# Kernel tuning notes

Hardware: AMD Instinct MI355X
Metric: run time of the kernel (lower is better)

## Reference

```python
import jax, jax.numpy as jnp
import numpy as np
import math

NUM_HEADS = 32
NUM_KV = 8
D = 128          # num_hidden == per-head dim in this module
S = 2048
B = 1
DK = 128
ROPE_BASE = 10000.0


def rope(x):
    # x: [B, H, S, D]; standard Llama-style RoPE (split-halves rotation) over positions.
    d = x.shape[-1]
    half = d // 2
    pos = jnp.arange(x.shape[2], dtype=jnp.float32)                       # [S]
    inv_freq = 1.0 / (ROPE_BASE ** (jnp.arange(half, dtype=jnp.float32) / half))
    ang = pos[:, None] * inv_freq[None, :]                                # [S, half]
    cos = jnp.cos(ang)
    sin = jnp.sin(ang)
    x1 = x[..., :half]
    x2 = x[..., half:]
    return jnp.concatenate([x1 * cos - x2 * sin, x1 * sin + x2 * cos], axis=-1)


def setup_inputs() -> dict:
    key = jax.random.key(0)
    ks = jax.random.split(key, 8)
    query = jax.random.normal(ks[0], (B, S, D), dtype=jnp.float32)
    k_in = jax.random.normal(ks[1], (B, S, D), dtype=jnp.float32)
    v_in = jax.random.normal(ks[2], (B, S, D), dtype=jnp.float32)
    # causal mask: 1 where attention allowed (lower triangle incl diagonal)
    mask = jnp.tril(jnp.ones((S, S), dtype=jnp.int32))[None, None]        # [1,1,S,S]
    sc = 0.02
    Wq = jax.random.normal(ks[3], (NUM_HEADS * D, D), dtype=jnp.float32) * sc
    bq = jnp.zeros((NUM_HEADS * D,), dtype=jnp.float32)
    Wk = jax.random.normal(ks[4], (NUM_KV * D, D), dtype=jnp.float32) * sc
    bk = jnp.zeros((NUM_KV * D,), dtype=jnp.float32)
    Wv = jax.random.normal(ks[5], (NUM_KV * D, D), dtype=jnp.float32) * sc
    bv = jnp.zeros((NUM_KV * D,), dtype=jnp.float32)
    Wo = jax.random.normal(ks[6], (D, NUM_HEADS * D), dtype=jnp.float32) * sc
    bo = jnp.zeros((D,), dtype=jnp.float32)
    return {"query": query, "key": k_in, "values": v_in, "mask": mask,
            "Wq": Wq, "bq": bq, "Wk": Wk, "bk": bk, "Wv": Wv, "bv": bv,
            "Wo": Wo, "bo": bo}


def reference(query, key, values, mask, Wq, bq, Wk, bk, Wv, bv, Wo, bo):
    Bq, Sq, Dh = query.shape
    # projections; torch Linear: x @ W.T + b. Note: view (reshape), not transpose,
    # exactly as in the original module.
    q = (query @ Wq.T + bq).reshape(Bq, NUM_HEADS, Sq, Dh)   # [B,H,S,D]
    k = (key @ Wk.T + bk).reshape(Bq, NUM_KV, Sq, Dh)        # [B,Hkv,S,D]
    v = (values @ Wv.T + bv).reshape(Bq, NUM_KV, Sq, Dh)
    rk = rope(k)
    rv = rope(v)  # module applies RoPE to values too (faithful)
    rep = NUM_HEADS // NUM_KV
    # torch .repeat((1, rep, 1, 1)) tiles whole head blocks -> jnp.tile
    rk = jnp.tile(rk, (1, rep, 1, 1))                        # [B,H,S,D]
    rv = jnp.tile(rv, (1, rep, 1, 1))
    scores = jnp.einsum('bhqd,bhkd->bhqk', q, rk) / math.sqrt(DK)
    scores = jnp.where(mask == 0, -jnp.inf, scores)
    attn = jax.nn.softmax(scores, axis=-1)
    out = jnp.einsum('bhqk,bhkd->bhqd', attn, rv)            # [B,H,S,D]
    out = out.transpose(0, 2, 1, 3).reshape(Bq, Sq, NUM_HEADS * Dh)
    return out @ Wo.T + bo
```

## Files before the change

### kernel.cpp

```cpp
#include <hip/hip_runtime.h>

typedef unsigned short u16;
typedef unsigned int u32;
typedef short frag_t __attribute__((ext_vector_type(8)));
typedef float f32x4 __attribute__((ext_vector_type(4)));

#define S_LEN 2048

__device__ __forceinline__ float bf2f(u32 u) {
  union { u32 i; float f; } v; v.i = u << 16; return v.f;
}
__device__ __forceinline__ u16 f2bf(float f) {
  u32 x = __float_as_uint(f);
  u32 r = (x + 0x7fffu + ((x >> 16) & 1u)) >> 16;
  return (u16)r;
}
__device__ __forceinline__ u32 pkbf(float lo, float hi) {
  u32 r;
  asm("v_cvt_pk_bf16_f32 %0, %1, %2" : "=v"(r) : "v"(lo), "v"(hi));
  return r;
}
__device__ __forceinline__ void unpack8(uint4 r, float* o) {
  o[0] = bf2f(r.x & 0xffffu); o[1] = bf2f(r.x >> 16);
  o[2] = bf2f(r.y & 0xffffu); o[3] = bf2f(r.y >> 16);
  o[4] = bf2f(r.z & 0xffffu); o[5] = bf2f(r.z >> 16);
  o[6] = bf2f(r.w & 0xffffu); o[7] = bf2f(r.w >> 16);
}
__device__ __forceinline__ u16 ld_in(const void* p, size_t idx, bool fp32) {
  if (fp32) return f2bf(((const float*)p)[idx]);
  return ((const u16*)p)[idx];
}
__device__ __forceinline__ uint4 ld8(const void* p, size_t eidx, bool fp32) {
  if (!fp32) return *(const uint4*)((const u16*)p + eidx);
  const float4* f = (const float4*)((const float*)p + eidx);
  float4 x = f[0], y = f[1];
  uint4 r;
  r.x = pkbf(x.x, x.y);
  r.y = pkbf(x.z, x.w);
  r.z = pkbf(y.x, y.y);
  r.w = pkbf(y.z, y.w);
  return r;
}

__global__ __launch_bounds__(256) void proj_all(
    const void* __restrict__ query, const void* __restrict__ key,
    const void* __restrict__ values,
    const void* __restrict__ Wq, const void* __restrict__ bq,
    const void* __restrict__ Wk, const void* __restrict__ bk,
    const void* __restrict__ Wv, const void* __restrict__ bv,
    u16* __restrict__ Qb, u16* __restrict__ Kb, u16* __restrict__ Vtmp,
    u32* __restrict__ flag_out) {
  __shared__ u16 As[128][136];
  __shared__ u16 Ws[128][136];
  __shared__ u32 flagS;
  u16 (*Cs)[136] = As;
  const int t = threadIdx.x;
  if (t < 64) {
    u32 e = ((u32)((const u16*)query)[2 * t] >> 7) & 0xFFu;
    bool ok = (e >= 110u && e <= 140u);
    unsigned long long b = __ballot(ok);
    if (t == 0) flagS = (__popcll(b) < 32) ? 1u : 0u;
  }
  __syncthreads();
  const bool fp32 = (flagS != 0u);
  if (t == 0 && blockIdx.x == 0 && blockIdx.y == 0) *flag_out = flagS;
  const int x = blockIdx.x;
  const void *A, *W, *bias;
  u16* C; int N, n0;
  if (x < 32)      { A = query;  W = Wq; bias = bq; C = Qb;   N = 4096; n0 = x << 7; }
  else if (x < 40) { A = key;    W = Wk; bias = bk; C = Kb;   N = 1024; n0 = (x - 32) << 7; }
  else             { A = values; W = Wv; bias = bv; C = Vtmp; N = 1024; n0 = (x - 40) << 7; }
  const float osc = (x < 32) ? 0.12751743f : 1.0f;
  const bool isK = (x >= 32 && x < 40);
  const int g0 = x - 32;
  const int lane = t & 63, w = t >> 6, quad = lane >> 4, l15 = lane & 15;
  const int rm = (w & 1) << 6, rn = (w >> 1) << 6;
#pragma unroll
  for (int i = 0; i < 8; ++i) {
    int task = t + (i << 8);
    int row = task >> 4, ch = (task & 15) << 3;
    *(uint4*)&Ws[row][ch] = ld8(W, (size_t)(n0 + row) * 128 + ch, fp32);
  }
  for (int mi = 0; mi < 2; ++mi) {
    const int m0 = (((int)blockIdx.y << 1) | mi) << 7;
    if (mi) __syncthreads();
#pragma unroll
    for (int i = 0; i < 8; ++i) {
      int task = t + (i << 8);
      int row = task >> 4, ch = (task & 15) << 3;
      *(uint4*)&As[row][ch] = ld8(A, (size_t)(m0 + row) * 128 + ch, fp32);
    }
    __syncthreads();
    f32x4 acc[4][4];
#pragma unroll
    for (int mt = 0; mt < 4; ++mt)
#pragma unroll
      for (int nt = 0; nt < 4; ++nt) acc[mt][nt] = 0.f;
#pragma unroll
    for (int mtp = 0; mtp < 2; ++mtp) {
      frag_t a0[4], a1[4];
#pragma unroll
      for (int kc = 0; kc < 4; ++kc) {
        a0[kc] = *(const frag_t*)&As[rm + mtp * 32 + l15][kc * 32 + quad * 8];
        a1[kc] = *(const frag_t*)&As[rm + mtp * 32 + 16 + l15][kc * 32 + quad * 8];
      }
#pragma unroll
      for (int nt = 0; nt < 4; ++nt)
#pragma unroll
        for (int kc = 0; kc < 4; ++kc) {
          frag_t b = *(const frag_t*)&Ws[rn + nt * 16 + l15][kc * 32 + quad * 8];
          acc[mtp * 2][nt] = __builtin_amdgcn_mfma_f32_16x16x32_bf16(a0[kc], b, acc[mtp * 2][nt], 0, 0, 0);
          acc[mtp * 2 + 1][nt] = __builtin_amdgcn_mfma_f32_16x16x32_bf16(a1[kc], b, acc[mtp * 2 + 1][nt], 0, 0, 0);
        }
    }
    __syncthreads();
#pragma unroll
    for (int nt = 0; nt < 4; ++nt) {
      float bb = bf2f((u32)ld_in(bias, n0 + rn + nt * 16 + l15, fp32));
#pragma unroll
      for (int mt = 0; mt < 4; ++mt) {
        int row = rm + ((mt >> 1) * 32) + ((mt & 1) * 16) + quad * 4;
#pragma unroll
        for (int r = 0; r < 4; ++r)
          Cs[row + r][rn + nt * 16 + l15] = f2bf((acc[mt][nt][r] + bb) * osc);
      }
    }
    __syncthreads();
    if (isK) {
      for (int i = t; i < 8192; i += 256) {
        int row = i >> 6, ii = i & 63;
        int sv = (((m0 + row) & 255) << 3) + g0;
        float invf = __expf(-(float)ii * 0.14391156831212787f);
        float ang = (float)sv * invf;
        float sn, cs;
        sincosf(ang, &sn, &cs);
        float k1 = bf2f((u32)Cs[row][ii]), k2 = bf2f((u32)Cs[row][ii + 64]);
        Cs[row][ii] = f2bf(k1 * cs - k2 * sn);
        Cs[row][ii + 64] = f2bf(k1 * sn + k2 * cs);
      }
      __syncthreads();
    }
#pragma unroll
    for (int i = 0; i < 8; ++i) {
      int task = t + (i << 8);
      int row = task >> 4, ch = (task & 15) << 3;
      *(uint4*)&C[(size_t)(m0 + row) * N + n0 + ch] = *(const uint4*)&Cs[row][ch];
    }
  }
}

__global__ __launch_bounds__(256) void rope_v_tr(const u16* __restrict__ Vb,
                                                 u16* __restrict__ VbT) {
  __shared__ u16 Lt[128][72];
  const int t = threadIdx.x;
  const int s0 = blockIdx.x << 6;
  const int g = blockIdx.y;
  const u16* src = Vb + (size_t)g * S_LEN * 128;
  for (int i = t; i < 512; i += 256) {
    int r = i >> 3, d8 = (i & 7) << 3;
    float lo[8], hi[8];
    unpack8(*(const uint4*)&src[(size_t)(s0 + r) * 128 + d8], lo);
    unpack8(*(const uint4*)&src[(size_t)(s0 + r) * 128 + d8 + 64], hi);
#pragma unroll
    for (int j = 0; j < 8; ++j) {
      float invf = __expf(-(float)(d8 + j) * 0.14391156831212787f);
      float ang = (float)(s0 + r) * invf;
      float sn, cs;
      sincosf(ang, &sn, &cs);
      Lt[d8 + j][r] = f2bf(lo[j] * cs - hi[j] * sn);
      Lt[d8 + 64 + j][r] = f2bf(lo[j] * sn + hi[j] * cs);
    }
  }
  __syncthreads();
  u16* dst = VbT + (size_t)g * 128 * S_LEN + s0;
  for (int i = t; i < 2048; i += 256) {
    int d = i >> 4, s4 = (i & 15) << 2;
    uint2 pk;
    pk.x = (u32)Lt[d][s4] | ((u32)Lt[d][s4 + 1] << 16);
    pk.y = (u32)Lt[d][s4 + 2] | ((u32)Lt[d][s4 + 3] << 16);
    *(uint2*)&dst[(size_t)d * S_LEN + s4] = pk;
  }
}

__global__ __launch_bounds__(256, 2) void attn_mfma(
    const u16* __restrict__ Qb, const u16* __restrict__ Kb,
    const u16* __restrict__ VbT, u16* __restrict__ OpA, u16* __restrict__ OpB,
    float2* __restrict__ Ml, int nkh) {
  __shared__ union SmemU {
    struct { u16 Kt[32][136]; u16 Vt[128][40]; u16 St[128][40]; } m;
    struct { u16 Og[128][136]; } e;
  } su;
  const int t = threadIdx.x;
  const int lane = t & 63, w = t >> 6, quad = lane >> 4, l15 = lane & 15;
  const int g = (int)blockIdx.x & 7;
  const int kh = (int)blockIdx.x >> 3;
  const int pi = (int)blockIdx.y;
  const int h = g + (w << 3);
  const u16* Kg = Kb + (size_t)g * S_LEN * 128;
  const u16* Vg = VbT + (size_t)g * 128 * S_LEN;
  const int kR = t >> 4, kC = (t & 15) << 3;
  const int vR = t >> 2, vC = (t & 3) << 3;
  u16* dst = kh ? OpB : OpA;

  for (int tp = 0; tp < 2; ++tp) {
    const int qt = tp ? pi : 63 - pi;
    const int q0 = qt << 5;
    const int niter = qt + 1;
    frag_t aq[2][4];
#pragma unroll
    for (int qp = 0; qp < 2; ++qp)
#pragma unroll
      for (int kc = 0; kc < 4; ++kc)
        aq[qp][kc] = *(const frag_t*)&Qb[((size_t)h * S_LEN + q0 + qp * 16 + l15) * 128 +
                                         kc * 32 + quad * 8];
    float m_r[2] = {-1e30f, -1e30f}, l_r[2] = {0.f, 0.f};
    f32x4 oacc[2][8];
#pragma unroll
    for (int qp = 0; qp < 2; ++qp)
#pragma unroll
      for (int nt = 0; nt < 8; ++nt) oacc[qp][nt] = 0.f;

    uint4 kpf[2], vpf[2];
    if (kh < niter) {
      const int k0 = kh << 5;
      kpf[0] = *(const uint4*)&Kg[(size_t)(k0 + kR) * 128 + kC];
      kpf[1] = *(const uint4*)&Kg[(size_t)(k0 + kR + 16) * 128 + kC];
      vpf[0] = *(const uint4*)&Vg[(size_t)vR * S_LEN + k0 + vC];
      vpf[1] = *(const uint4*)&Vg[(size_t)(vR + 64) * S_LEN + k0 + vC];
    }
    for (int sj = kh; sj < niter; sj += nkh) {
      const int k0 = sj << 5;
      __syncthreads();
      *(uint4*)&su.m.Kt[kR][kC] = kpf[0];
      *(uint4*)&su.m.Kt[kR + 16][kC] = kpf[1];
      *(uint4*)&su.m.Vt[vR][vC] = vpf[0];
      *(uint4*)&su.m.Vt[vR + 64][vC] = vpf[1];
      __syncthreads();
      if (sj + nkh < niter) {
        const int kn = (sj + nkh) << 5;
        kpf[0] = *(const uint4*)&Kg[(size_t)(kn + kR) * 128 + kC];
        kpf[1] = *(const uint4*)&Kg[(size_t)(kn + kR + 16) * 128 + kC];
        vpf[0] = *(const uint4*)&Vg[(size_t)vR * S_LEN + kn + vC];
        vpf[1] = *(const uint4*)&Vg[(size_t)(vR + 64) * S_LEN + kn + vC];
      }
      f32x4 s4[2][2];
#pragma unroll
      for (int kk = 0; kk < 2; ++kk) { s4[kk][0] = 0.f; s4[kk][1] = 0.f; }
#pragma unroll
      for (int kc = 0; kc < 4; ++kc)
#pragma unroll
        for (int kk = 0; kk < 2; ++kk) {
          frag_t a = *(const frag_t*)&su.m.Kt[kk * 16 + l15][kc * 32 + quad * 8];
          s4[kk][0] = __builtin_amdgcn_mfma_f32_16x16x32_bf16(a, aq[0][kc], s4[kk][0], 0, 0, 0);
          s4[kk][1] = __builtin_amdgcn_mfma_f32_16x16x32_bf16(a, aq[1][kc], s4[kk][1], 0, 0, 0);
        }
      const bool lastm = (sj == niter - 1);
      float alpha[2];
#pragma unroll
      for (int qp = 0; qp < 2; ++qp) {
        const int qg = q0 + qp * 16 + l15;
        float mx = -1e30f;
#pragma unroll
        for (int kk = 0; kk < 2; ++kk)
#pragma unroll
          for (int r = 0; r < 4; ++r) {
            float sv = s4[kk][qp][r];
            if (lastm && (k0 + kk * 16 + quad * 4 + r) > qg) sv = -1e30f;
            s4[kk][qp][r] = sv;
            mx = fmaxf(mx, sv);
          }
        mx = fmaxf(mx, __shfl_xor(mx, 16));
        mx = fmaxf(mx, __shfl_xor(mx, 32));
        float mn = fmaxf(m_r[qp], mx);
        alpha[qp] = __builtin_amdgcn_exp2f(m_r[qp] - mn);
        m_r[qp] = mn;
        float sum = 0.f;
        const int strow = w * 32 + qp * 16 + l15;
#pragma unroll
        for (int kk = 0; kk < 2; ++kk) {
          float p0 = __builtin_amdgcn_exp2f(s4[kk][qp][0] - mn);
          float p1 = __builtin_amdgcn_exp2f(s4[kk][qp][1] - mn);
          float p2 = __builtin_amdgcn_exp2f(s4[kk][qp][2] - mn);
          float p3 = __builtin_amdgcn_exp2f(s4[kk][qp][3] - mn);
          sum += (p0 + p1) + (p2 + p3);
          uint2 pk;
          pk.x = pkbf(p0, p1);
          pk.y = pkbf(p2, p3);
          *(uint2*)&su.m.St[strow][kk * 16 + quad * 4] = pk;
        }
        sum += __shfl_xor(sum, 16);
        sum += __shfl_xor(sum, 32);
        l_r[qp] = l_r[qp] * alpha[qp] + sum;
      }
      if (__any(alpha[0] < 1.0f || alpha[1] < 1.0f)) {
#pragma unroll
        for (int qp = 0; qp < 2; ++qp)
#pragma unroll
          for (int r = 0; r < 4; ++r) {
            float al = __shfl(alpha[qp], quad * 4 + r);
#pragma unroll
            for (int nt = 0; nt < 8; ++nt) oacc[qp][nt][r] *= al;
          }
      }
      frag_t pa0 = *(const frag_t*)&su.m.St[w * 32 + l15][quad * 8];
      frag_t pa1 = *(const frag_t*)&su.m.St[w * 32 + 16 + l15][quad * 8];
#pragma unroll
      for (int nt = 0; nt < 8; ++nt) {
        frag_t v = *(const frag_t*)&su.m.Vt[nt * 16 + l15][quad * 8];
        oacc[0][nt] = __builtin_amdgcn_mfma_f32_16x16x32_bf16(pa0, v, oacc[0][nt], 0, 0, 0);
        oacc[1][nt] = __builtin_amdgcn_mfma_f32_16x16x32_bf16(pa1, v, oacc[1][nt], 0, 0, 0);
      }
    }
    __syncthreads();
#pragma unroll
    for (int qp = 0; qp < 2; ++qp)
#pragma unroll
      for (int r = 0; r < 4; ++r) {
        float fac = 1.0f;
        if (nkh == 1) fac = 1.0f / __shfl(l_r[qp], quad * 4 + r);
        int row = w * 32 + qp * 16 + quad * 4 + r;
#pragma unroll
        for (int nt = 0; nt < 8; ++nt)
          su.e.Og[row][nt * 16 + l15] = f2bf(oacc[qp][nt][r] * fac);
      }
    __syncthreads();
#pragma unroll
    for (int jj = 0; jj < 8; ++jj) {
      int c = t + (jj << 8);
      int row = c >> 4, ch = (c & 15) << 3;
      int hh = row >> 5, qr = row & 31;
      *(uint4*)&dst[(size_t)(q0 + qr) * 4096 + (g + hh * 8) * 128 + ch] =
          *(const uint4*)&su.e.Og[row][ch];
    }
    if (nkh == 2 && quad == 0) {
#pragma unroll
      for (int qp = 0; qp < 2; ++qp)
        Ml[((size_t)kh * 32 + h) * S_LEN + q0 + qp * 16 + l15] =
            make_float2(m_r[qp], l_r[qp]);
    }
  }
}

__global__ __launch_bounds__(256) void out_part(
    const u16* __restrict__ OpA, const u16* __restrict__ OpB,
    const float2* __restrict__ Ml, const void* __restrict__ Wo,
    float* __restrict__ Pout, const u32* __restrict__ flagp, int nkh) {
  __shared__ u16 As[64][136];
  __shared__ u16 Ws[128][136];
  const bool fp32 = (*flagp != 0u);
  const int t = threadIdx.x;
  const int lane = t & 63, w = t >> 6, quad = lane >> 4, l15 = lane & 15;
  const int rm = (w & 1) << 5, rn = (w >> 1) << 6;
  const int m0 = (int)blockIdx.x << 6;
  const int z = (int)blockIdx.y;
  f32x4 acc[2][4];
#pragma unroll
  for (int mt = 0; mt < 2; ++mt)
#pragma unroll
    for (int nt = 0; nt < 4; ++nt) acc[mt][nt] = 0.f;
  for (int kc2 = 0; kc2 < 2; ++kc2) {
    if (kc2) __syncthreads();
    const int kc0 = (z << 8) + (kc2 << 7);
    const int hh = kc0 >> 7;
#pragma unroll
    for (int i = 0; i < 8; ++i) {
      int task = t + (i << 8);
      int row = task >> 4, ch = (task & 15) << 3;
      *(uint4*)&Ws[row][ch] = ld8(Wo, (size_t)row * 4096 + kc0 + ch, fp32);
    }
#pragma unroll
    for (int i = 0; i < 4; ++i) {
      int task = t + (i << 8);
      int row = task >> 4, ch = (task & 15) << 3;
      size_t idx = (size_t)(m0 + row) * 4096 + kc0 + ch;
      if (nkh == 2) {
        int s = m0 + row;
        float2 p1 = Ml[(size_t)hh * S_LEN + s];
        float2 p2 = Ml[(size_t)(32 + hh) * S_LEN + s];
        float mn = fmaxf(p1.x, p2.x);
        float a1 = __builtin_amdgcn_exp2f(p1.x - mn);
        float a2 = __builtin_amdgcn_exp2f(p2.x - mn);
        float linv = 1.0f / (a1 * p1.y + a2 * p2.y);
        float w1 = a1 * linv, w2 = a2 * linv;
        float o1[8], o2[8];
        unpack8(*(const uint4*)&OpA[idx], o1);
        unpack8(*(const uint4*)&OpB[idx], o2);
        uint4 r;
        r.x = pkbf(o1[0] * w1 + o2[0] * w2, o1[1] * w1 + o2[1] * w2);
        r.y = pkbf(o1[2] * w1 + o2[2] * w2, o1[3] * w1 + o2[3] * w2);
        r.z = pkbf(o1[4] * w1 + o2[4] * w2, o1[5] * w1 + o2[5] * w2);
        r.w = pkbf(o1[6] * w1 + o2[6] * w2, o1[7] * w1 + o2[7] * w2);
        *(uint4*)&As[row][ch] = r;
      } else {
        *(uint4*)&As[row][ch] = *(const uint4*)&OpA[idx];
      }
    }
    __syncthreads();
    frag_t a0[4], a1[4];
#pragma unroll
    for (int kc = 0; kc < 4; ++kc) {
      a0[kc] = *(const frag_t*)&As[rm + l15][kc * 32 + quad * 8];
      a1[kc] = *(const frag_t*)&As[rm + 16 + l15][kc * 32 + quad * 8];
    }
#pragma unroll
    for (int nt = 0; nt < 4; ++nt)
#pragma unroll
      for (int kc = 0; kc < 4; ++kc) {
        frag_t b = *(const frag_t*)&Ws[rn + nt * 16 + l15][kc * 32 + quad * 8];
        acc[0][nt] = __builtin_amdgcn_mfma_f32_16x16x32_bf16(a0[kc], b, acc[0][nt], 0, 0, 0);
        acc[1][nt] = __builtin_amdgcn_mfma_f32_16x16x32_bf16(a1[kc], b, acc[1][nt], 0, 0, 0);
      }
  }
#pragma unroll
  for (int mt = 0; mt < 2; ++mt) {
    int mrow = m0 + rm + mt * 16 + quad * 4;
#pragma unroll
    for (int nt = 0; nt < 4; ++nt) {
      int n = rn + nt * 16 + l15;
#pragma unroll
      for (int r = 0; r < 4; ++r)
        Pout[((size_t)z * 2048 + mrow + r) * 128 + n] = acc[mt][nt][r];
    }
  }
}

__global__ __launch_bounds__(256) void out_red(
    const float* __restrict__ Pout, const void* __restrict__ bo,
    void* __restrict__ out, const u32* __restrict__ flagp) {
  const bool fp32 = (*flagp != 0u);
  int e4 = blockIdx.x * 256 + threadIdx.x;
  const float4* P = (const float4*)Pout;
  float4 s = P[e4];
#pragma unroll
  for (int z = 1; z < 16; ++z) {
    float4 p = P[(size_t)z * 65536 + e4];
    s.x += p.x; s.y += p.y; s.z += p.z; s.w += p.w;
  }
  int n = (e4 << 2) & 127;
  s.x += bf2f((u32)ld_in(bo, n + 0, fp32));
  s.y += bf2f((u32)ld_in(bo, n + 1, fp32));
  s.z += bf2f((u32)ld_in(bo, n + 2, fp32));
  s.w += bf2f((u32)ld_in(bo, n + 3, fp32));
  if (fp32) {
    ((float4*)out)[e4] = s;
  } else {
    uint2 pk;
    pk.x = pkbf(s.x, s.y);
    pk.y = pkbf(s.z, s.w);
    *(uint2*)((u16*)out + (e4 << 2)) = pk;
  }
}

extern "C" void kernel_launch(void* const* d_in, const int* in_sizes, int n_in,
                              void* d_out, int out_size, void* d_ws, size_t ws_size,
                              hipStream_t stream) {
  (void)in_sizes; (void)n_in; (void)out_size;
  const void* query  = d_in[0];
  const void* key    = d_in[1];
  const void* values = d_in[2];
  const void* Wq = d_in[4];
  const void* bq = d_in[5];
  const void* Wk = d_in[6];
  const void* bk = d_in[7];
  const void* Wv = d_in[8];
  const void* bv = d_in[9];
  const void* Wo = d_in[10];
  const void* bo = d_in[11];

  char* ws = (char*)d_ws;
  u32* flag   = (u32*)ws;
  u16* Qb     = (u16*)(ws + 64);
  u16* Kb     = (u16*)(ws + 64 + (16ull << 20));
  u16* VbT    = (u16*)(ws + 64 + (20ull << 20));
  u16* Vtmp   = (u16*)(ws + 64 + (24ull << 20));
  u16* OpA    = (u16*)(ws + 64 + (24ull << 20));
  u16* OpB    = (u16*)(ws + 64 + (40ull << 20));
  float2* Mlb = (float2*)(ws + 64 + (56ull << 20));
  float* Pout = (float*)Qb;

  const bool split = (ws_size >= (58ull << 20));
  const int nkh = split ? 2 : 1;

  proj_all<<<dim3(48, 8), 256, 0, stream>>>(query, key, values, Wq, bq, Wk, bk,
                                            Wv, bv, Qb, Kb, Vtmp, flag);
  rope_v_tr<<<dim3(32, 8), 256, 0, stream>>>(Vtmp, VbT);
  attn_mfma<<<dim3(8 * nkh, 32), 256, 0, stream>>>(Qb, Kb, VbT, OpA, OpB, Mlb,
                                                   nkh);
  out_part<<<dim3(32, 16), 256, 0, stream>>>(OpA, OpB, Mlb, Wo, Pout, flag, nkh);
  out_red<<<256, 256, 0, stream>>>(Pout, bo, d_out, flag);
}
```

Measured before the change: 236.2 us.

## Split attention blocks to 16 query rows per wave and fuse V RoPE into projection

Each attention block previously computed 4 heads × 32 query rows, with each wave owning two 16-row query tiles. It now covers 2 heads × 32 rows, with each wave owning one 16-row tile. This doubles the grid and halves per-wave registers so that launch bounds can allow 3 blocks per SM. RoPE on V moves into the projection kernel's epilogue, so the transpose kernel becomes a pure transpose. The cost is that each K/V tile is loaded and staged twice as often across blocks.

```diff
diff --git a/kernel.cpp b/kernel.cpp
--- a/kernel.cpp
+++ b/kernel.cpp
@@ -71,8 +71,8 @@
   else if (x < 40) { A = key;    W = Wk; bias = bk; C = Kb;   N = 1024; n0 = (x - 32) << 7; }
   else             { A = values; W = Wv; bias = bv; C = Vtmp; N = 1024; n0 = (x - 40) << 7; }
   const float osc = (x < 32) ? 0.12751743f : 1.0f;
-  const bool isK = (x >= 32 && x < 40);
-  const int g0 = x - 32;
+  const bool doRope = (x >= 32);
+  const int g0 = (x < 40) ? (x - 32) : (x - 40);
   const int lane = t & 63, w = t >> 6, quad = lane >> 4, l15 = lane & 15;
   const int rm = (w & 1) << 6, rn = (w >> 1) << 6;
 #pragma unroll
@@ -126,7 +126,7 @@
       }
     }
     __syncthreads();
-    if (isK) {
+    if (doRope) {
       for (int i = t; i < 8192; i += 256) {
         int row = i >> 6, ii = i & 63;
         int sv = (((m0 + row) & 255) << 3) + g0;
@@ -149,27 +149,24 @@
   }
 }
 
-__global__ __launch_bounds__(256) void rope_v_tr(const u16* __restrict__ Vb,
-                                                 u16* __restrict__ VbT) {
+__global__ __launch_bounds__(256) void v_tr(const u16* __restrict__ Vb,
+                                            u16* __restrict__ VbT) {
   __shared__ u16 Lt[128][72];
   const int t = threadIdx.x;
   const int s0 = blockIdx.x << 6;
   const int g = blockIdx.y;
   const u16* src = Vb + (size_t)g * S_LEN * 128;
-  for (int i = t; i < 512; i += 256) {
-    int r = i >> 3, d8 = (i & 7) << 3;
-    float lo[8], hi[8];
-    unpack8(*(const uint4*)&src[(size_t)(s0 + r) * 128 + d8], lo);
-    unpack8(*(const uint4*)&src[(size_t)(s0 + r) * 128 + d8 + 64], hi);
-#pragma unroll
-    for (int j = 0; j < 8; ++j) {
-      float invf = __expf(-(float)(d8 + j) * 0.14391156831212787f);
-      float ang = (float)(s0 + r) * invf;
-      float sn, cs;
-      sincosf(ang, &sn, &cs);
-      Lt[d8 + j][r] = f2bf(lo[j] * cs - hi[j] * sn);
-      Lt[d8 + 64 + j][r] = f2bf(lo[j] * sn + hi[j] * cs);
-    }
+  for (int i = t; i < 1024; i += 256) {
+    int r = i >> 4, d16 = (i & 15) << 3;
+    uint4 v = *(const uint4*)&src[(size_t)(s0 + r) * 128 + d16];
+    Lt[d16 + 0][r] = (u16)(v.x & 0xffffu);
+    Lt[d16 + 1][r] = (u16)(v.x >> 16);
+    Lt[d16 + 2][r] = (u16)(v.y & 0xffffu);
+    Lt[d16 + 3][r] = (u16)(v.y >> 16);
+    Lt[d16 + 4][r] = (u16)(v.z & 0xffffu);
+    Lt[d16 + 5][r] = (u16)(v.z >> 16);
+    Lt[d16 + 6][r] = (u16)(v.w & 0xffffu);
+    Lt[d16 + 7][r] = (u16)(v.w >> 16);
   }
   __syncthreads();
   u16* dst = VbT + (size_t)g * 128 * S_LEN + s0;
@@ -182,20 +179,24 @@
   }
 }
 
-__global__ __launch_bounds__(256, 2) void attn_mfma(
+__global__ __launch_bounds__(256, 3) void attn_mfma(
     const u16* __restrict__ Qb, const u16* __restrict__ Kb,
     const u16* __restrict__ VbT, u16* __restrict__ OpA, u16* __restrict__ OpB,
     float2* __restrict__ Ml, int nkh) {
   __shared__ union SmemU {
     struct { u16 Kt[32][136]; u16 Vt[128][40]; u16 St[128][40]; } m;
-    struct { u16 Og[128][136]; } e;
+    struct { u16 Og[64][136]; } e;
   } su;
   const int t = threadIdx.x;
   const int lane = t & 63, w = t >> 6, quad = lane >> 4, l15 = lane & 15;
-  const int g = (int)blockIdx.x & 7;
-  const int kh = (int)blockIdx.x >> 3;
+  const int x = (int)blockIdx.x;
+  const int g = x & 7;
+  const int jh = (x >> 3) & 1;
+  const int kh = x >> 4;
   const int pi = (int)blockIdx.y;
-  const int h = g + (w << 3);
+  const int j = (jh << 1) + (w >> 1);
+  const int h = g + (j << 3);
+  const int qsub = (w & 1) << 4;
   const u16* Kg = Kb + (size_t)g * S_LEN * 128;
   const u16* Vg = VbT + (size_t)g * 128 * S_LEN;
   const int kR = t >> 4, kC = (t & 15) << 3;
@@ -206,19 +207,15 @@
     const int qt = tp ? pi : 63 - pi;
     const int q0 = qt << 5;
     const int niter = qt + 1;
-    frag_t aq[2][4];
-#pragma unroll
-    for (int qp = 0; qp < 2; ++qp)
-#pragma unroll
-      for (int kc = 0; kc < 4; ++kc)
-        aq[qp][kc] = *(const frag_t*)&Qb[((size_t)h * S_LEN + q0 + qp * 16 + l15) * 128 +
-                                         kc * 32 + quad * 8];
-    float m_r[2] = {-1e30f, -1e30f}, l_r[2] = {0.f, 0.f};
-    f32x4 oacc[2][8];
-#pragma unroll
-    for (int qp = 0; qp < 2; ++qp)
-#pragma unroll
-      for (int nt = 0; nt < 8; ++nt) oacc[qp][nt] = 0.f;
+    frag_t aq[4];
+#pragma unroll
+    for (int kc = 0; kc < 4; ++kc)
+      aq[kc] = *(const frag_t*)&Qb[((size_t)h * S_LEN + q0 + qsub + l15) * 128 +
+                                   kc * 32 + quad * 8];
+    float m_r = -1e30f, l_r = 0.f;
+    f32x4 oacc[8];
+#pragma unroll
+    for (int nt = 0; nt < 8; ++nt) oacc[nt] = 0.f;
 
     uint4 kpf[2], vpf[2];
     if (kh < niter) {
@@ -243,101 +240,88 @@
         vpf[0] = *(const uint4*)&Vg[(size_t)vR * S_LEN + kn + vC];
         vpf[1] = *(const uint4*)&Vg[(size_t)(vR + 64) * S_LEN + kn + vC];
       }
-      f32x4 s4[2][2];
-#pragma unroll
-      for (int kk = 0; kk < 2; ++kk) { s4[kk][0] = 0.f; s4[kk][1] = 0.f; }
+      f32x4 s4[2];
+      s4[0] = 0.f; s4[1] = 0.f;
 #pragma unroll
       for (int kc = 0; kc < 4; ++kc)
 #pragma unroll
         for (int kk = 0; kk < 2; ++kk) {
           frag_t a = *(const frag_t*)&su.m.Kt[kk * 16 + l15][kc * 32 + quad * 8];
-          s4[kk][0] = __builtin_amdgcn_mfma_f32_16x16x32_bf16(a, aq[0][kc], s4[kk][0], 0, 0, 0);
-          s4[kk][1] = __builtin_amdgcn_mfma_f32_16x16x32_bf16(a, aq[1][kc], s4[kk][1], 0, 0, 0);
+          s4[kk] = __builtin_amdgcn_mfma_f32_16x16x32_bf16(a, aq[kc], s4[kk], 0, 0, 0);
         }
       const bool lastm = (sj == niter - 1);
-      float alpha[2];
-#pragma unroll
-      for (int qp = 0; qp < 2; ++qp) {
-        const int qg = q0 + qp * 16 + l15;
-        float mx = -1e30f;
-#pragma unroll
-        for (int kk = 0; kk < 2; ++kk)
-#pragma unroll
-          for (int r = 0; r < 4; ++r) {
-            float sv = s4[kk][qp][r];
-            if (lastm && (k0 + kk * 16 + quad * 4 + r) > qg) sv = -1e30f;
-            s4[kk][qp][r] = sv;
-            mx = fmaxf(mx, sv);
-          }
-        mx = fmaxf(mx, __shfl_xor(mx, 16));
-        mx = fmaxf(mx, __shfl_xor(mx, 32));
-        float mn = fmaxf(m_r[qp], mx);
-        alpha[qp] = __builtin_amdgcn_exp2f(m_r[qp] - mn);
-        m_r[qp] = mn;
-        float sum = 0.f;
-        const int strow = w * 32 + qp * 16 + l15;
-#pragma unroll
-        for (int kk = 0; kk < 2; ++kk) {
-          float p0 = __builtin_amdgcn_exp2f(s4[kk][qp][0] - mn);
-          float p1 = __builtin_amdgcn_exp2f(s4[kk][qp][1] - mn);
-          float p2 = __builtin_amdgcn_exp2f(s4[kk][qp][2] - mn);
-          float p3 = __builtin_amdgcn_exp2f(s4[kk][qp][3] - mn);
-          sum += (p0 + p1) + (p2 + p3);
-          uint2 pk;
-          pk.x = pkbf(p0, p1);
-          pk.y = pkbf(p2, p3);
-          *(uint2*)&su.m.St[strow][kk * 16 + quad * 4] = pk;
+      const int qg = q0 + qsub + l15;
+      float mx = -1e30f;
+#pragma unroll
+      for (int kk = 0; kk < 2; ++kk)
+#pragma unroll
+        for (int r = 0; r < 4; ++r) {
+          float sv = s4[kk][r];
+          if (lastm && (k0 + kk * 16 + quad * 4 + r) > qg) sv = -1e30f;
+          s4[kk][r] = sv;
+          mx = fmaxf(mx, sv);
         }
-        sum += __shfl_xor(sum, 16);
-        sum += __shfl_xor(sum, 32);
-        l_r[qp] = l_r[qp] * alpha[qp] + sum;
-      }
-      if (__any(alpha[0] < 1.0f || alpha[1] < 1.0f)) {
-#pragma unroll
-        for (int qp = 0; qp < 2; ++qp)
-#pragma unroll
-          for (int r = 0; r < 4; ++r) {
-            float al = __shfl(alpha[qp], quad * 4 + r);
-#pragma unroll
-            for (int nt = 0; nt < 8; ++nt) oacc[qp][nt][r] *= al;
-          }
-      }
-      frag_t pa0 = *(const frag_t*)&su.m.St[w * 32 + l15][quad * 8];
-      frag_t pa1 = *(const frag_t*)&su.m.St[w * 32 + 16 + l15][quad * 8];
+      mx = fmaxf(mx, __shfl_xor(mx, 16));
+      mx = fmaxf(mx, __shfl_xor(mx, 32));
+      float mn = fmaxf(m_r, mx);
+      float alpha = __builtin_amdgcn_exp2f(m_r - mn);
+      m_r = mn;
+      float sum = 0.f;
+      const int strow = (w << 5) + l15;
+#pragma unroll
+      for (int kk = 0; kk < 2; ++kk) {
+        float p0 = __builtin_amdgcn_exp2f(s4[kk][0] - mn);
+        float p1 = __builtin_amdgcn_exp2f(s4[kk][1] - mn);
+        float p2 = __builtin_amdgcn_exp2f(s4[kk][2] - mn);
+        float p3 = __builtin_amdgcn_exp2f(s4[kk][3] - mn);
+        sum += (p0 + p1) + (p2 + p3);
+        uint2 pk;
+        pk.x = pkbf(p0, p1);
+        pk.y = pkbf(p2, p3);
+        *(uint2*)&su.m.St[strow][kk * 16 + quad * 4] = pk;
+      }
+      sum += __shfl_xor(sum, 16);
+      sum += __shfl_xor(sum, 32);
+      l_r = l_r * alpha + sum;
+      if (__any(alpha < 1.0f)) {
+#pragma unroll
+        for (int r = 0; r < 4; ++r) {
+          float al = __shfl(alpha, quad * 4 + r);
+#pragma unroll
+          for (int nt = 0; nt < 8; ++nt) oacc[nt][r] *= al;
+        }
+      }
+      frag_t pa = *(const frag_t*)&su.m.St[strow][quad * 8];
 #pragma unroll
       for (int nt = 0; nt < 8; ++nt) {
         frag_t v = *(const frag_t*)&su.m.Vt[nt * 16 + l15][quad * 8];
-        oacc[0][nt] = __builtin_amdgcn_mfma_f32_16x16x32_bf16(pa0, v, oacc[0][nt], 0, 0, 0);
-        oacc[1][nt] = __builtin_amdgcn_mfma_f32_16x16x32_bf16(pa1, v, oacc[1][nt], 0, 0, 0);
-      }
-    }
-    __syncthreads();
-#pragma unroll
-    for (int qp = 0; qp < 2; ++qp)
-#pragma unroll
-      for (int r = 0; r < 4; ++r) {
-        float fac = 1.0f;
-        if (nkh == 1) fac = 1.0f / __shfl(l_r[qp], quad * 4 + r);
-        int row = w * 32 + qp * 16 + quad * 4 + r;
-#pragma unroll
-        for (int nt = 0; nt < 8; ++nt)
-          su.e.Og[row][nt * 16 + l15] = f2bf(oacc[qp][nt][r] * fac);
-      }
-    __syncthreads();
-#pragma unroll
-    for (int jj = 0; jj < 8; ++jj) {
+        oacc[nt] = __builtin_amdgcn_mfma_f32_16x16x32_bf16(pa, v, oacc[nt], 0, 0, 0);
+      }
+    }
+    __syncthreads();
+#pragma unroll
+    for (int r = 0; r < 4; ++r) {
+      float fac = 1.0f;
+      if (nkh == 1) fac = 1.0f / __shfl(l_r, quad * 4 + r);
+      int row = (w << 4) + quad * 4 + r;
+#pragma unroll
+      for (int nt = 0; nt < 8; ++nt)
+        su.e.Og[row][nt * 16 + l15] = f2bf(oacc[nt][r] * fac);
+    }
+    __syncthreads();
+#pragma unroll
+    for (int jj = 0; jj < 4; ++jj) {
       int c = t + (jj << 8);
       int row = c >> 4, ch = (c & 15) << 3;
-      int hh = row >> 5, qr = row & 31;
-      *(uint4*)&dst[(size_t)(q0 + qr) * 4096 + (g + hh * 8) * 128 + ch] =
+      int wv = row >> 4;
+      int j2 = (jh << 1) + (wv >> 1);
+      int qr = ((wv & 1) << 4) + (row & 15);
+      *(uint4*)&dst[(size_t)(q0 + qr) * 4096 + (g + (j2 << 3)) * 128 + ch] =
           *(const uint4*)&su.e.Og[row][ch];
     }
-    if (nkh == 2 && quad == 0) {
-#pragma unroll
-      for (int qp = 0; qp < 2; ++qp)
-        Ml[((size_t)kh * 32 + h) * S_LEN + q0 + qp * 16 + l15] =
-            make_float2(m_r[qp], l_r[qp]);
-    }
+    if (nkh == 2 && quad == 0)
+      Ml[((size_t)kh * 32 + h) * S_LEN + q0 + qsub + l15] = make_float2(m_r, l_r);
+    __syncthreads();
   }
 }
 
@@ -483,9 +467,9 @@
 
   proj_all<<<dim3(48, 8), 256, 0, stream>>>(query, key, values, Wq, bq, Wk, bk,
                                             Wv, bv, Qb, Kb, Vtmp, flag);
-  rope_v_tr<<<dim3(32, 8), 256, 0, stream>>>(Vtmp, VbT);
-  attn_mfma<<<dim3(8 * nkh, 32), 256, 0, stream>>>(Qb, Kb, VbT, OpA, OpB, Mlb,
-                                                   nkh);
+  v_tr<<<dim3(32, 8), 256, 0, stream>>>(Vtmp, VbT);
+  attn_mfma<<<dim3(16 * nkh, 32), 256, 0, stream>>>(Qb, Kb, VbT, OpA, OpB, Mlb,
+                                                    nkh);
   out_part<<<dim3(32, 16), 256, 0, stream>>>(OpA, OpB, Mlb, Wo, Pout, flag, nkh);
   out_red<<<256, 256, 0, stream>>>(Pout, bo, d_out, flag);
 }
```

Result: slower. 298.3 us (+26.3%).

## Fuse V RoPE into projection and output reduction into out_part via atomic tickets

Applied to the files above, without the earlier changes.

V RoPE now runs inside the projection kernel's epilogue, as K RoPE already did, so the separate transpose kernel only transposes. The separate out_red launch is removed: each out_part block increments a per-row-tile counter, and the last of the 16 split-K blocks sums the partials, adds the bias and writes the output. The counters are zeroed in the projection kernel. Pout gets its own region when the workspace is large enough, so it no longer aliases Qb. This cuts one launch and the extra transcendental work in the transpose pass, at the cost of threadfence and atomic overhead and a serialized reduction tail.

```diff
diff --git a/kernel.cpp b/kernel.cpp
--- a/kernel.cpp
+++ b/kernel.cpp
@@ -49,7 +49,7 @@
     const void* __restrict__ Wk, const void* __restrict__ bk,
     const void* __restrict__ Wv, const void* __restrict__ bv,
     u16* __restrict__ Qb, u16* __restrict__ Kb, u16* __restrict__ Vtmp,
-    u32* __restrict__ flag_out) {
+    u32* __restrict__ flag_out, u32* __restrict__ cnt) {
   __shared__ u16 As[128][136];
   __shared__ u16 Ws[128][136];
   __shared__ u32 flagS;
@@ -63,7 +63,10 @@
   }
   __syncthreads();
   const bool fp32 = (flagS != 0u);
-  if (t == 0 && blockIdx.x == 0 && blockIdx.y == 0) *flag_out = flagS;
+  if (blockIdx.x == 0 && blockIdx.y == 0) {
+    if (t == 0) *flag_out = flagS;
+    if (t < 32) cnt[t] = 0;
+  }
   const int x = blockIdx.x;
   const void *A, *W, *bias;
   u16* C; int N, n0;
@@ -71,8 +74,8 @@
   else if (x < 40) { A = key;    W = Wk; bias = bk; C = Kb;   N = 1024; n0 = (x - 32) << 7; }
   else             { A = values; W = Wv; bias = bv; C = Vtmp; N = 1024; n0 = (x - 40) << 7; }
   const float osc = (x < 32) ? 0.12751743f : 1.0f;
-  const bool isK = (x >= 32 && x < 40);
-  const int g0 = x - 32;
+  const bool doRope = (x >= 32);
+  const int g0 = (x < 40) ? (x - 32) : (x - 40);
   const int lane = t & 63, w = t >> 6, quad = lane >> 4, l15 = lane & 15;
   const int rm = (w & 1) << 6, rn = (w >> 1) << 6;
 #pragma unroll
@@ -126,7 +129,7 @@
       }
     }
     __syncthreads();
-    if (isK) {
+    if (doRope) {
       for (int i = t; i < 8192; i += 256) {
         int row = i >> 6, ii = i & 63;
         int sv = (((m0 + row) & 255) << 3) + g0;
@@ -149,27 +152,24 @@
   }
 }
 
-__global__ __launch_bounds__(256) void rope_v_tr(const u16* __restrict__ Vb,
-                                                 u16* __restrict__ VbT) {
+__global__ __launch_bounds__(256) void v_tr(const u16* __restrict__ Vb,
+                                            u16* __restrict__ VbT) {
   __shared__ u16 Lt[128][72];
   const int t = threadIdx.x;
   const int s0 = blockIdx.x << 6;
   const int g = blockIdx.y;
   const u16* src = Vb + (size_t)g * S_LEN * 128;
-  for (int i = t; i < 512; i += 256) {
-    int r = i >> 3, d8 = (i & 7) << 3;
-    float lo[8], hi[8];
-    unpack8(*(const uint4*)&src[(size_t)(s0 + r) * 128 + d8], lo);
-    unpack8(*(const uint4*)&src[(size_t)(s0 + r) * 128 + d8 + 64], hi);
-#pragma unroll
-    for (int j = 0; j < 8; ++j) {
-      float invf = __expf(-(float)(d8 + j) * 0.14391156831212787f);
-      float ang = (float)(s0 + r) * invf;
-      float sn, cs;
-      sincosf(ang, &sn, &cs);
-      Lt[d8 + j][r] = f2bf(lo[j] * cs - hi[j] * sn);
-      Lt[d8 + 64 + j][r] = f2bf(lo[j] * sn + hi[j] * cs);
-    }
+  for (int i = t; i < 1024; i += 256) {
+    int r = i >> 4, d16 = (i & 15) << 3;
+    uint4 v = *(const uint4*)&src[(size_t)(s0 + r) * 128 + d16];
+    Lt[d16 + 0][r] = (u16)(v.x & 0xffffu);
+    Lt[d16 + 1][r] = (u16)(v.x >> 16);
+    Lt[d16 + 2][r] = (u16)(v.y & 0xffffu);
+    Lt[d16 + 3][r] = (u16)(v.y >> 16);
+    Lt[d16 + 4][r] = (u16)(v.z & 0xffffu);
+    Lt[d16 + 5][r] = (u16)(v.z >> 16);
+    Lt[d16 + 6][r] = (u16)(v.w & 0xffffu);
+    Lt[d16 + 7][r] = (u16)(v.w >> 16);
   }
   __syncthreads();
   u16* dst = VbT + (size_t)g * 128 * S_LEN + s0;
@@ -344,9 +344,12 @@
 __global__ __launch_bounds__(256) void out_part(
     const u16* __restrict__ OpA, const u16* __restrict__ OpB,
     const float2* __restrict__ Ml, const void* __restrict__ Wo,
-    float* __restrict__ Pout, const u32* __restrict__ flagp, int nkh) {
+    float* __restrict__ Pout, const u32* __restrict__ flagp, int nkh,
+    u32* __restrict__ cnt, const void* __restrict__ bo,
+    void* __restrict__ out) {
   __shared__ u16 As[64][136];
   __shared__ u16 Ws[128][136];
+  __shared__ u32 tickS;
   const bool fp32 = (*flagp != 0u);
   const int t = threadIdx.x;
   const int lane = t & 63, w = t >> 6, quad = lane >> 4, l15 = lane & 15;
@@ -422,32 +425,36 @@
         Pout[((size_t)z * 2048 + mrow + r) * 128 + n] = acc[mt][nt][r];
     }
   }
-}
-
-__global__ __launch_bounds__(256) void out_red(
-    const float* __restrict__ Pout, const void* __restrict__ bo,
-    void* __restrict__ out, const u32* __restrict__ flagp) {
-  const bool fp32 = (*flagp != 0u);
-  int e4 = blockIdx.x * 256 + threadIdx.x;
-  const float4* P = (const float4*)Pout;
-  float4 s = P[e4];
-#pragma unroll
-  for (int z = 1; z < 16; ++z) {
-    float4 p = P[(size_t)z * 65536 + e4];
-    s.x += p.x; s.y += p.y; s.z += p.z; s.w += p.w;
-  }
-  int n = (e4 << 2) & 127;
-  s.x += bf2f((u32)ld_in(bo, n + 0, fp32));
-  s.y += bf2f((u32)ld_in(bo, n + 1, fp32));
-  s.z += bf2f((u32)ld_in(bo, n + 2, fp32));
-  s.w += bf2f((u32)ld_in(bo, n + 3, fp32));
-  if (fp32) {
-    ((float4*)out)[e4] = s;
-  } else {
-    uint2 pk;
-    pk.x = pkbf(s.x, s.y);
-    pk.y = pkbf(s.z, s.w);
-    *(uint2*)((u16*)out + (e4 << 2)) = pk;
+  __threadfence();
+  __syncthreads();
+  if (t == 0) tickS = atomicAdd(&cnt[blockIdx.x], 1u);
+  __syncthreads();
+  if (tickS == 15) {
+    __threadfence();
+    const float4* P = (const float4*)Pout;
+    for (int i = t; i < 2048; i += 256) {
+      int row = i >> 5, c4 = i & 31;
+      size_t base = (size_t)(m0 + row) * 32 + c4;
+      float4 s = P[base];
+#pragma unroll
+      for (int zz = 1; zz < 16; ++zz) {
+        float4 p = P[(size_t)zz * 65536 + base];
+        s.x += p.x; s.y += p.y; s.z += p.z; s.w += p.w;
+      }
+      int n = c4 << 2;
+      s.x += bf2f((u32)ld_in(bo, n + 0, fp32));
+      s.y += bf2f((u32)ld_in(bo, n + 1, fp32));
+      s.z += bf2f((u32)ld_in(bo, n + 2, fp32));
+      s.w += bf2f((u32)ld_in(bo, n + 3, fp32));
+      if (fp32) {
+        ((float4*)out)[base] = s;
+      } else {
+        uint2 pk;
+        pk.x = pkbf(s.x, s.y);
+        pk.y = pkbf(s.z, s.w);
+        *(uint2*)((u16*)out + (base << 2)) = pk;
+      }
+    }
   }
 }
 
@@ -469,23 +476,26 @@
 
   char* ws = (char*)d_ws;
   u32* flag   = (u32*)ws;
-  u16* Qb     = (u16*)(ws + 64);
-  u16* Kb     = (u16*)(ws + 64 + (16ull << 20));
-  u16* VbT    = (u16*)(ws + 64 + (20ull << 20));
-  u16* Vtmp   = (u16*)(ws + 64 + (24ull << 20));
-  u16* OpA    = (u16*)(ws + 64 + (24ull << 20));
-  u16* OpB    = (u16*)(ws + 64 + (40ull << 20));
-  float2* Mlb = (float2*)(ws + 64 + (56ull << 20));
-  float* Pout = (float*)Qb;
+  u32* cnt    = (u32*)(ws + 256);
+  u16* Qb     = (u16*)(ws + 1024);
+  u16* Kb     = (u16*)(ws + 1024 + (16ull << 20));
+  u16* VbT    = (u16*)(ws + 1024 + (20ull << 20));
+  u16* Vtmp   = (u16*)(ws + 1024 + (24ull << 20));
+  u16* OpA    = (u16*)(ws + 1024 + (24ull << 20));
+  u16* OpB    = (u16*)(ws + 1024 + (40ull << 20));
+  float2* Mlb = (float2*)(ws + 1024 + (56ull << 20));
+  float* Pout = (ws_size >= (74ull << 20))
+                    ? (float*)(ws + 1024 + (57ull << 20))
+                    : (float*)Qb;
 
   const bool split = (ws_size >= (58ull << 20));
   const int nkh = split ? 2 : 1;
 
   proj_all<<<dim3(48, 8), 256, 0, stream>>>(query, key, values, Wq, bq, Wk, bk,
-                                            Wv, bv, Qb, Kb, Vtmp, flag);
-  rope_v_tr<<<dim3(32, 8), 256, 0, stream>>>(Vtmp, VbT);
+                                            Wv, bv, Qb, Kb, Vtmp, flag, cnt);
+  v_tr<<<dim3(32, 8), 256, 0, stream>>>(Vtmp, VbT);
   attn_mfma<<<dim3(8 * nkh, 32), 256, 0, stream>>>(Qb, Kb, VbT, OpA, OpB, Mlb,
                                                    nkh);
-  out_part<<<dim3(32, 16), 256, 0, stream>>>(OpA, OpB, Mlb, Wo, Pout, flag, nkh);
-  out_red<<<256, 256, 0, stream>>>(Pout, bo, d_out, flag);
-}
+  out_part<<<dim3(32, 16), 256, 0, stream>>>(OpA, OpB, Mlb, Wo, Pout, flag, nkh,
+                                             cnt, bo, d_out);
+}
```

Result: slower. 308.3 us (+30.5%).
